# Kernel optimization log

Hardware: AMD Instinct MI355X
Metric: run time of the kernel (lower is better)

Reference implementation:

```python
import jax, jax.numpy as jnp
import numpy as np

S, B, C, H, DH = 16, 16, 256, 4, 64
HW_TABLE, HW_HAND = 256, 36
HW = HW_TABLE + HW_HAND + 1  # 293 spatial tokens (table + hand + global)
LK = 128
MAX_T = 64
UH, UW, UC = 4, 4, 2
TH, TW, HH, HWW = 16, 16, 6, 6
N_MODES, N_SHAPES, N_COLORS = 20, 64, 16


def _ln(x, g, b):
    m = jnp.mean(x, -1, keepdims=True)
    v = jnp.var(x, -1, keepdims=True)
    return (x - m) / jnp.sqrt(v + 1e-5) * g + b


def _forward(tq, pad_q, xk, tk, pad_k,
             spatial_enc, temporal_enc, ln1_g, ln1_b,
             wq, bq, wk, bk, wv, bv, wo, bo, ln2_g, ln2_b,
             w1, b1, w2, b2, table_w, table_b, hand_w, hand_b,
             mode_w, mode_b, shape_w, shape_b, color_w, color_b):
    s, b = tq.shape
    Lq = s * HW
    # temporal + spatial positional broadcast-add -> padded query stream
    xt = temporal_enc[tq]                                        # (s,b,C)
    xq = (xt[:, None] + spatial_enc[None, :, None]).reshape(Lq, b, C)
    tq_e = jnp.broadcast_to(tq[:, None], (s, HW, b)).reshape(Lq, b)
    # padded causal mask: key visible iff tk <= tq, key in pad_k, query in pad_q*HW
    allowed = ((tk[None] <= tq_e[:, None])
               & (jnp.arange(LK)[None, :, None] < pad_k[None, None])
               & (jnp.arange(Lq)[:, None, None] < (pad_q * HW)[None, None]))  # (Lq,Lk,b)
    # cross-attention TransformerBlock (pre-LN MHA + FFN)
    qn = _ln(xq, ln1_g, ln1_b)
    Q = (qn @ wq + bq).reshape(Lq, b, H, DH)
    K = (xk @ wk + bk).reshape(LK, b, H, DH)
    V = (xk @ wv + bv).reshape(LK, b, H, DH)
    scores = jnp.einsum('qbhd,kbhd->bhqk', Q, K) / np.float32(np.sqrt(DH))
    scores = jnp.where(jnp.transpose(allowed, (2, 0, 1))[:, None], scores, jnp.float32(-1e9))
    a = jnp.einsum('bhqk,kbhd->qbhd', jax.nn.softmax(scores, -1), V).reshape(Lq, b, C)
    x = xq + a @ wo + bo
    x = x + jax.nn.gelu(_ln(x, ln2_g, ln2_b) @ w1 + b1) @ w2 + b2
    x = x.reshape(s, HW, b, C)
    # table decode: pixel-unshuffle (s,th,tw,b,uh,uw,uc) -> (s,b,uc,th*uh,tw*uw)
    tx = x[:, :HW_TABLE] @ table_w + table_b
    tx = tx.reshape(s, TH, TW, b, UH, UW, UC).transpose(0, 3, 6, 1, 4, 2, 5)
    tx = tx.reshape(s, b, UC, TH * UH, TW * UW)
    hx = x[:, HW_TABLE:HW_TABLE + HW_HAND] @ hand_w + hand_b
    hx = hx.reshape(s, HH, HWW, b, UH, UW, UC).transpose(0, 3, 6, 1, 4, 2, 5)
    hx = hx.reshape(s, b, UC, HH * UH, HWW * UW)
    gx = x[:, HW - 1]  # (s,b,C) global token
    return (gx @ mode_w + mode_b, gx @ shape_w + shape_b, gx @ color_w + color_b, tx, hx)


def setup_inputs():
    ks = jax.random.split(jax.random.key(0), 40)
    p = lambda k, shp: jax.random.normal(k, shp, jnp.float32) * 0.02
    inp = {}
    inp['tq'] = jnp.sort(jax.random.randint(ks[0], (S, B), 0, MAX_T), axis=0)
    inp['pad_q'] = jax.random.randint(ks[1], (B,), S // 2, S + 1)
    inp['xk'] = jax.random.normal(ks[2], (LK, B, C), jnp.float32)
    inp['tk'] = jnp.sort(jax.random.randint(ks[3], (LK, B), 0, MAX_T), axis=0).at[0].set(0)
    inp['pad_k'] = jax.random.randint(ks[4], (B,), LK // 2, LK + 1)
    inp['table_cursor_activate'] = jax.random.randint(ks[5], (S, B), 0, 2)
    inp['hand_cursor_activate'] = jax.random.randint(ks[6], (S, B), 0, 2)
    inp['insert_activate'] = jax.random.randint(ks[7], (S, B), 0, 2)
    inp['spatial_enc'] = p(ks[8], (HW, C))
    inp['temporal_enc'] = p(ks[9], (MAX_T, C))
    inp['ln1_g'] = jnp.ones(C); inp['ln1_b'] = jnp.zeros(C)
    inp['wq'] = p(ks[10], (C, C)); inp['bq'] = jnp.zeros(C)
    inp['wk'] = p(ks[11], (C, C)); inp['bk'] = jnp.zeros(C)
    inp['wv'] = p(ks[12], (C, C)); inp['bv'] = jnp.zeros(C)
    inp['wo'] = p(ks[13], (C, C)); inp['bo'] = jnp.zeros(C)
    inp['ln2_g'] = jnp.ones(C); inp['ln2_b'] = jnp.zeros(C)
    inp['w1'] = p(ks[14], (C, 4 * C)); inp['b1'] = jnp.zeros(4 * C)
    inp['w2'] = p(ks[15], (4 * C, C)); inp['b2'] = jnp.zeros(C)
    inp['table_w'] = p(ks[16], (C, UH * UW * UC)); inp['table_b'] = jnp.zeros(UH * UW * UC)
    inp['hand_w'] = p(ks[17], (C, UH * UW * UC)); inp['hand_b'] = jnp.zeros(UH * UW * UC)
    inp['mode_w'] = p(ks[18], (C, N_MODES)); inp['mode_b'] = jnp.zeros(N_MODES)
    inp['shape_w'] = p(ks[19], (C, N_SHAPES)); inp['shape_b'] = jnp.zeros(N_SHAPES)
    inp['color_w'] = p(ks[20], (C, N_COLORS)); inp['color_b'] = jnp.zeros(N_COLORS)
    return inp


def reference(tq, pad_q, xk, tk, pad_k, table_cursor_activate, hand_cursor_activate,
              insert_activate, spatial_enc, temporal_enc, ln1_g, ln1_b,
              wq, bq, wk, bk, wv, bv, wo, bo, ln2_g, ln2_b,
              w1, b1, w2, b2, table_w, table_b, hand_w, hand_b,
              mode_w, mode_b, shape_w, shape_b, color_w, color_b):
    # cursor/insert activates are unused in the old_style branch
    return _forward(tq, pad_q, xk, tk, pad_k, spatial_enc, temporal_enc,
                    ln1_g, ln1_b, wq, bq, wk, bk, wv, bv, wo, bo, ln2_g, ln2_b,
                    w1, b1, w2, b2, table_w, table_b, hand_w, hand_b,
                    mode_w, mode_b, shape_w, shape_b, color_w, color_b)
```

## Files before the change

### kernel.cpp

```cpp
#include <hip/hip_runtime.h>
#include <hip/hip_bf16.h>

namespace {
constexpr int cS = 16, cB = 16, cC = 256, cH = 4, cDH = 64, cHW = 293;
constexpr int cLQ = cS * cHW;
constexpr int cLK = 128;
constexpr int cNN = cLQ * cB;
constexpr size_t TX_OFF = 25600;
constexpr size_t HX_OFF = 2122752;
}

typedef unsigned short ushort_t;
typedef unsigned int uint_t;
typedef __attribute__((ext_vector_type(8))) short short8;
typedef __attribute__((ext_vector_type(4))) float f32x4;

__device__ __forceinline__ float bf2f(ushort_t u) {
  return __uint_as_float(((uint_t)u) << 16);
}
__device__ __forceinline__ ushort_t f2bf(float f) {
  __hip_bfloat16 h = __float2bfloat16(f);
  return *(ushort_t*)&h;
}

__device__ __forceinline__ size_t swz(int r, int c) {
  return (((size_t)(r >> 4) * 8 + (c >> 5)) * 64 + ((c >> 3) & 3) * 16 + (r & 15)) * 8 + (c & 7);
}

__global__ __launch_bounds__(256) void k_prep(
    const float* __restrict__ xk, ushort_t* __restrict__ xkb,
    const float* __restrict__ wq, ushort_t* __restrict__ wqs,
    const float* __restrict__ wk, ushort_t* __restrict__ wks,
    const float* __restrict__ wv, ushort_t* __restrict__ wvs,
    const float* __restrict__ wo, ushort_t* __restrict__ wos,
    const float* __restrict__ w1, ushort_t* __restrict__ w1s,
    const float* __restrict__ w2, ushort_t* __restrict__ w2s,
    const float* __restrict__ tw, ushort_t* __restrict__ tws,
    const float* __restrict__ hw_, ushort_t* __restrict__ hws)
{
  int bid = blockIdx.x;
  if (bid < 512) {
    int i4 = bid * 256 + threadIdx.x;
    int r = i4 >> 6;
    int c0 = (i4 & 63) * 4;
    float4 v = *(const float4*)(xk + (size_t)r * 256 + c0);
    ushort_t o[4] = {f2bf(v.x), f2bf(v.y), f2bf(v.z), f2bf(v.w)};
    *(uint2*)&xkb[swz(r, c0)] = *(uint2*)o;
    return;
  }
  int rr = bid - 512;
  const float* W; ushort_t* Ws; int N; int lb;
  if      (rr < 32)  { W = wq;  Ws = wqs; N = 256;  lb = rr; }
  else if (rr < 64)  { W = wk;  Ws = wks; N = 256;  lb = rr - 32; }
  else if (rr < 96)  { W = wv;  Ws = wvs; N = 256;  lb = rr - 64; }
  else if (rr < 128) { W = wo;  Ws = wos; N = 256;  lb = rr - 96; }
  else if (rr < 256) { W = w1;  Ws = w1s; N = 1024; lb = rr - 128; }
  else if (rr < 384) { W = w2;  Ws = w2s; N = 256;  lb = rr - 256; }
  else if (rr < 388) { W = tw;  Ws = tws; N = 32;   lb = rr - 384; }
  else               { W = hw_; Ws = hws; N = 32;   lb = rr - 388; }
  int slot = lb * 256 + threadIdx.x;
  int lane = slot & 63;
  int fr   = slot >> 6;
  int NB   = N >> 4;
  int nb   = fr % NB, kc = fr / NB;
  int n    = nb * 16 + (lane & 15);
  int k0   = kc * 32 + (lane >> 4) * 8;
  ushort_t tmp[8];
  #pragma unroll
  for (int i = 0; i < 8; ++i) tmp[i] = f2bf(W[(size_t)(k0 + i) * N + n]);
  *(uint4*)&Ws[(size_t)slot * 8] = *(uint4*)tmp;
}

__device__ __forceinline__ void gemm_k256(
    const ushort_t* __restrict__ A, const ushort_t* __restrict__ Ws,
    int rt0, int slot0, int NB, int lane, f32x4 c[4][4])
{
  #pragma unroll 2
  for (int kc = 0; kc < 8; ++kc) {
    short8 a[4];
    #pragma unroll
    for (int mf = 0; mf < 4; ++mf)
      a[mf] = *(const short8*)(A + (((size_t)(rt0 + mf) * 8 + kc) * 64 + lane) * 8);
    #pragma unroll
    for (int nb = 0; nb < 4; ++nb) {
      short8 b = *(const short8*)(Ws + (((size_t)kc * NB + slot0 + nb) * 64 + lane) * 8);
      #pragma unroll
      for (int mf = 0; mf < 4; ++mf)
        c[mf][nb] = __builtin_amdgcn_mfma_f32_16x16x32_bf16(a[mf], b, c[mf][nb], 0, 0, 0);
    }
  }
}

__global__ __launch_bounds__(256, 4) void k_qnp(
    const int* __restrict__ tq, const float* __restrict__ spatial,
    const float* __restrict__ temporal, const float* __restrict__ g,
    const float* __restrict__ bt, const ushort_t* __restrict__ Ws,
    const float* __restrict__ Bi, ushort_t* __restrict__ Out)
{
  __shared__ ushort_t aT[64 * 256];
  const int tid = threadIdx.x, lane = tid & 63, w = tid >> 6;
  const int rt0 = blockIdx.x * 4, row0 = blockIdx.x * 64;
  {
    int q = rt0 + w;
    int s = q / cHW, hw = q % cHW;
    int c0 = lane * 4;
    float4 sv = *(const float4*)(spatial + (size_t)hw * cC + c0);
    float4 g4 = *(const float4*)(g + c0);
    float4 b4 = *(const float4*)(bt + c0);
    int kc = c0 >> 5, qq = (c0 >> 3) & 3, joff = c0 & 7;
    for (int rr = 0; rr < 16; ++rr) {
      int t = tq[s * cB + rr];
      float4 tv = *(const float4*)(temporal + (size_t)t * cC + c0);
      float v0 = tv.x + sv.x, v1 = tv.y + sv.y, v2 = tv.z + sv.z, v3 = tv.w + sv.w;
      float sum = v0 + v1 + v2 + v3;
      float sum2 = v0 * v0 + v1 * v1 + v2 * v2 + v3 * v3;
      #pragma unroll
      for (int off = 32; off >= 1; off >>= 1) {
        sum  += __shfl_xor(sum,  off, 64);
        sum2 += __shfl_xor(sum2, off, 64);
      }
      float mean = sum * (1.0f / cC);
      float var  = sum2 * (1.0f / cC) - mean * mean;
      float inv  = rsqrtf(var + 1e-5f);
      ushort_t o[4] = {f2bf((v0 - mean) * inv * g4.x + b4.x),
                       f2bf((v1 - mean) * inv * g4.y + b4.y),
                       f2bf((v2 - mean) * inv * g4.z + b4.z),
                       f2bf((v3 - mean) * inv * g4.w + b4.w)};
      *(uint2*)&aT[(((w * 8 + kc) * 64) + qq * 16 + rr) * 8 + joff] = *(uint2*)o;
    }
  }
  __syncthreads();
  f32x4 z = {0.f, 0.f, 0.f, 0.f};
  f32x4 c[4][4];
  #pragma unroll
  for (int mf = 0; mf < 4; ++mf)
    #pragma unroll
    for (int nb = 0; nb < 4; ++nb) c[mf][nb] = z;
  gemm_k256(aT, Ws, 0, w * 4, 16, lane, c);
  const int lane15 = lane & 15, kq = lane >> 4;
  __syncthreads();
  #pragma unroll
  for (int nb = 0; nb < 4; ++nb) {
    int col = w * 64 + nb * 16 + lane15;
    float bias = Bi[col];
    #pragma unroll
    for (int mf = 0; mf < 4; ++mf)
      #pragma unroll
      for (int i = 0; i < 4; ++i)
        aT[(mf * 16 + kq * 4 + i) * 256 + col] = f2bf(c[mf][nb][i] + bias);
  }
  __syncthreads();
  uint2* outp = (uint2*)(Out + (size_t)row0 * 256);
  #pragma unroll
  for (int it = 0; it < 16; ++it) {
    int f = tid + it * 256;
    int row = f >> 6, c0 = (f & 63) * 4;
    outp[f] = *(uint2*)&aT[row * 256 + c0];
  }
}

__global__ __launch_bounds__(256, 4) void k_kv(
    const ushort_t* __restrict__ xkb, const ushort_t* __restrict__ wks,
    const ushort_t* __restrict__ wvs, const float* __restrict__ bk,
    const float* __restrict__ bv, ushort_t* __restrict__ Kb,
    ushort_t* __restrict__ Vb)
{
  const ushort_t* Ws = blockIdx.y ? wvs : wks;
  const float* Bi = blockIdx.y ? bv : bk;
  ushort_t* Out = blockIdx.y ? Vb : Kb;
  const int lane = threadIdx.x & 63, w = threadIdx.x >> 6;
  const int rt0 = blockIdx.x * 4, row0 = blockIdx.x * 64;
  f32x4 z = {0.f, 0.f, 0.f, 0.f};
  f32x4 c[4][4];
  #pragma unroll
  for (int mf = 0; mf < 4; ++mf)
    #pragma unroll
    for (int nb = 0; nb < 4; ++nb) c[mf][nb] = z;
  gemm_k256(xkb, Ws, rt0, w * 4, 16, lane, c);
  const int lane15 = lane & 15, kq = lane >> 4;
  #pragma unroll
  for (int nb = 0; nb < 4; ++nb) {
    int col = w * 64 + nb * 16 + lane15;
    float bias = Bi[col];
    #pragma unroll
    for (int mf = 0; mf < 4; ++mf)
      #pragma unroll
      for (int i = 0; i < 4; ++i) {
        int row = row0 + mf * 16 + kq * 4 + i;
        Out[(size_t)row * 256 + col] = f2bf(c[mf][nb][i] + bias);
      }
  }
}

__global__ __launch_bounds__(512, 4) void k_woffn(
    const ushort_t* __restrict__ A, const ushort_t* __restrict__ wos,
    const float* __restrict__ bo, const int* __restrict__ tq,
    const float* __restrict__ spatial, const float* __restrict__ temporal,
    const float* __restrict__ g, const float* __restrict__ bt,
    const ushort_t* __restrict__ w1s, const float* __restrict__ b1,
    const ushort_t* __restrict__ w2s, const float* __restrict__ b2,
    ushort_t* xres, ushort_t* __restrict__ x2out)
{
  __shared__ ushort_t aT[64 * 256];
  __shared__ ushort_t hL[64 * 256];
  __shared__ float red[8][64][2];
  __shared__ float meanL[64], invL[64];
  const int tid = threadIdx.x, lane = tid & 63, w = tid >> 6;
  const int lane15 = lane & 15, kq = lane >> 4;
  const int rt0 = blockIdx.x * 4, row0 = blockIdx.x * 64;
  const f32x4 z = {0.f, 0.f, 0.f, 0.f};

  f32x4 c[4][2];
  #pragma unroll
  for (int mf = 0; mf < 4; ++mf)
    #pragma unroll
    for (int nb = 0; nb < 2; ++nb) c[mf][nb] = z;
  #pragma unroll 1
  for (int kc = 0; kc < 8; ++kc) {
    short8 a[4];
    #pragma unroll
    for (int mf = 0; mf < 4; ++mf)
      a[mf] = *(const short8*)(A + (((size_t)(rt0 + mf) * 8 + kc) * 64 + lane) * 8);
    #pragma unroll
    for (int nb = 0; nb < 2; ++nb) {
      short8 b = *(const short8*)(wos + (((size_t)kc * 16 + w * 2 + nb) * 64 + lane) * 8);
      #pragma unroll
      for (int mf = 0; mf < 4; ++mf)
        c[mf][nb] = __builtin_amdgcn_mfma_f32_16x16x32_bf16(a[mf], b, c[mf][nb], 0, 0, 0);
    }
  }
  {
    int tt[4][4], hws[4];
    #pragma unroll
    for (int mf = 0; mf < 4; ++mf) {
      int q = rt0 + mf;
      int s = q / cHW;
      hws[mf] = q % cHW;
      #pragma unroll
      for (int i = 0; i < 4; ++i) tt[mf][i] = tq[s * cB + kq * 4 + i];
    }
    #pragma unroll
    for (int nb = 0; nb < 2; ++nb) {
      int col = w * 32 + nb * 16 + lane15;
      float bias = bo[col];
      #pragma unroll
      for (int mf = 0; mf < 4; ++mf) {
        float sp = spatial[(size_t)hws[mf] * cC + col];
        #pragma unroll
        for (int i = 0; i < 4; ++i)
          c[mf][nb][i] += bias + temporal[(size_t)tt[mf][i] * cC + col] + sp;
      }
    }
  }
  #pragma unroll
  for (int mf = 0; mf < 4; ++mf)
    #pragma unroll
    for (int i = 0; i < 4; ++i) {
      float s4 = c[mf][0][i] + c[mf][1][i];
      float q4 = c[mf][0][i] * c[mf][0][i] + c[mf][1][i] * c[mf][1][i];
      #pragma unroll
      for (int off = 8; off >= 1; off >>= 1) {
        s4 += __shfl_xor(s4, off, 64);
        q4 += __shfl_xor(q4, off, 64);
      }
      if (lane15 == 0) {
        red[w][mf * 16 + kq * 4 + i][0] = s4;
        red[w][mf * 16 + kq * 4 + i][1] = q4;
      }
    }
  __syncthreads();
  if (tid < 64) {
    float S = 0.f, Q = 0.f;
    #pragma unroll
    for (int ww = 0; ww < 8; ++ww) { S += red[ww][tid][0]; Q += red[ww][tid][1]; }
    float m = S * (1.0f / cC);
    float v = Q * (1.0f / cC) - m * m;
    meanL[tid] = m;
    invL[tid] = rsqrtf(v + 1e-5f);
  }
  __syncthreads();
  #pragma unroll
  for (int nb = 0; nb < 2; ++nb) {
    int col = w * 32 + nb * 16 + lane15;
    float gc = g[col], bc = bt[col];
    int qd = nb * 2 + (lane15 >> 3);
    int jd = lane15 & 7;
    #pragma unroll
    for (int mf = 0; mf < 4; ++mf)
      #pragma unroll
      for (int i = 0; i < 4; ++i) {
        int rl = mf * 16 + kq * 4 + i;
        float val = c[mf][nb][i];
        float lv = (val - meanL[rl]) * invL[rl] * gc + bc;
        aT[((mf * 8 + w) * 64 + qd * 16 + kq * 4 + i) * 8 + jd] = f2bf(lv);
        hL[rl * 256 + col] = f2bf(val);
      }
  }
  __syncthreads();
  {
    uint2* xw = (uint2*)(xres + (size_t)row0 * 256);
    #pragma unroll
    for (int it = 0; it < 8; ++it) {
      int f = tid + it * 512;
      int row = f >> 6, c0 = (f & 63) * 4;
      xw[f] = *(uint2*)&hL[row * 256 + c0];
    }
  }
  f32x4 c2[4][2];
  #pragma unroll
  for (int mf = 0; mf < 4; ++mf)
    #pragma unroll
    for (int nb = 0; nb < 2; ++nb) c2[mf][nb] = z;
  for (int hc = 0; hc < 4; ++hc) {
    #pragma unroll
    for (int half = 0; half < 2; ++half) {
      f32x4 c1[4];
      #pragma unroll
      for (int mf = 0; mf < 4; ++mf) c1[mf] = z;
      #pragma unroll 1
      for (int kc = 0; kc < 8; ++kc) {
        short8 a[4];
        #pragma unroll
        for (int mf = 0; mf < 4; ++mf)
          a[mf] = *(const short8*)&aT[((mf * 8 + kc) * 64 + lane) * 8];
        int slot = hc * 16 + w * 2 + half;
        short8 b = *(const short8*)(w1s + (((size_t)kc * 64 + slot) * 64 + lane) * 8);
        #pragma unroll
        for (int mf = 0; mf < 4; ++mf)
          c1[mf] = __builtin_amdgcn_mfma_f32_16x16x32_bf16(a[mf], b, c1[mf], 0, 0, 0);
      }
      if (half == 0) __syncthreads();
      {
        int k2l = w * 32 + half * 16 + lane15;
        float bias = b1[hc * 256 + k2l];
        int kc2l = k2l >> 5, kq2 = (k2l >> 3) & 3, j2 = k2l & 7;
        #pragma unroll
        for (int mf = 0; mf < 4; ++mf)
          #pragma unroll
          for (int i = 0; i < 4; ++i) {
            float xx = c1[mf][i] + bias;
            float x2v = xx * xx;
            float mm = fmaf(x2v, 0.044715f, 1.0f);
            float u2 = xx * mm * -1.5957691216057308f;
            float e = __expf(u2);
            float ge = xx * __builtin_amdgcn_rcpf(1.0f + e);
            hL[(((kc2l * 4 + mf) * 64) + kq2 * 16 + kq * 4 + i) * 8 + j2] = f2bf(ge);
          }
      }
    }
    __syncthreads();
    #pragma unroll 1
    for (int kc2 = 0; kc2 < 8; ++kc2) {
      short8 a2[4];
      #pragma unroll
      for (int mf = 0; mf < 4; ++mf)
        a2[mf] = *(const short8*)&hL[((kc2 * 4 + mf) * 64 + lane) * 8];
      #pragma unroll
      for (int nb = 0; nb < 2; ++nb) {
        short8 b = *(const short8*)(w2s +
            (((size_t)(hc * 8 + kc2) * 16 + w * 2 + nb) * 64 + lane) * 8);
        #pragma unroll
        for (int mf = 0; mf < 4; ++mf)
          c2[mf][nb] = __builtin_amdgcn_mfma_f32_16x16x32_bf16(a2[mf], b, c2[mf][nb], 0, 0, 0);
      }
    }
  }
  __syncthreads();
  #pragma unroll
  for (int nb = 0; nb < 2; ++nb) {
    int col = w * 32 + nb * 16 + lane15;
    float bias = b2[col];
    #pragma unroll
    for (int mf = 0; mf < 4; ++mf)
      #pragma unroll
      for (int i = 0; i < 4; ++i)
        aT[(mf * 16 + kq * 4 + i) * 256 + col] = f2bf(c2[mf][nb][i] + bias);
  }
  __syncthreads();
  {
    const int rt = (tid + 256) & 511;
    uint2* xp = (uint2*)(x2out + (size_t)row0 * 256);
    const uint2* xr = (const uint2*)(xres + (size_t)row0 * 256);
    #pragma unroll
    for (int it = 0; it < 8; ++it) {
      int f = rt + it * 512;
      int row = f >> 6, c0 = (f & 63) * 4;
      uint2 hv = *(uint2*)&aT[row * 256 + c0];
      uint2 rv = xr[f];
      const ushort_t* hp = (const ushort_t*)&hv;
      const ushort_t* rp = (const ushort_t*)&rv;
      ushort_t o[4];
      #pragma unroll
      for (int j = 0; j < 4; ++j) o[j] = f2bf(bf2f(hp[j]) + bf2f(rp[j]));
      xp[f] = *(uint2*)o;
    }
  }
}

__global__ __launch_bounds__(512, 4) void k_attn(
    const ushort_t* __restrict__ Qb, const ushort_t* __restrict__ Kb,
    const ushort_t* __restrict__ Vb, const int* __restrict__ tq,
    const int* __restrict__ tk, const int* __restrict__ pad_q,
    const int* __restrict__ pad_k, ushort_t* __restrict__ aout)
{
  __shared__ ushort_t KL[128 * 72];
  __shared__ ushort_t VtL[64 * 136];
  __shared__ ushort_t pL[8][16 * 136];
  __shared__ int tkL[128];

  const int h = blockIdx.y, b = blockIdx.z;
  const int tid = threadIdx.x, lane = tid & 63, w = tid >> 6;
  const int m15 = lane & 15, quad = lane >> 4;

  for (int i = tid; i < 128 * 16; i += 512) {
    int k = i >> 4, d4 = (i & 15) * 4;
    size_t src = (size_t)(k * cB + b) * 256 + h * 64 + d4;
    uint2 kv = *(const uint2*)&Kb[src];
    uint2 vv = *(const uint2*)&Vb[src];
    *(uint2*)&KL[k * 72 + d4] = kv;
    const ushort_t* vvp = (const ushort_t*)&vv;
    #pragma unroll
    for (int t = 0; t < 4; ++t) VtL[(d4 + t) * 136 + k] = vvp[t];
  }
  if (tid < 128) tkL[tid] = tk[tid * cB + b];
  __syncthreads();
  const int pk = pad_k[b];
  const int pq = pad_q[b] * cHW;
  ushort_t* pRow = pL[w];
  const f32x4 z = {0.f, 0.f, 0.f, 0.f};

  for (int pr = 0; pr < 4; ++pr) {
    int qt = blockIdx.x * 32 + pr * 8 + w;
    if (qt >= 293) break;
    const ushort_t* qrow =
        Qb + ((size_t)((qt * 16 + m15) * cB + b)) * 256 + h * 64 + quad * 8;
    short8 qa0 = *(const short8*)(qrow);
    short8 qa1 = *(const short8*)(qrow + 32);
    f32x4 s[8];
    #pragma unroll
    for (int nf = 0; nf < 8; ++nf) {
      const ushort_t* kp = KL + (nf * 16 + m15) * 72 + quad * 8;
      short8 b0 = *(const short8*)(kp);
      short8 b1 = *(const short8*)(kp + 32);
      s[nf] = __builtin_amdgcn_mfma_f32_16x16x32_bf16(qa0, b0, z, 0, 0, 0);
      s[nf] = __builtin_amdgcn_mfma_f32_16x16x32_bf16(qa1, b1, s[nf], 0, 0, 0);
    }
    int tqv[4], qok[4];
    #pragma unroll
    for (int i = 0; i < 4; ++i) {
      int qg = qt * 16 + quad * 4 + i;
      int sidx = (qg * 3579) >> 20;
      tqv[i] = tq[sidx * cB + b];
      qok[i] = (qg < pq);
    }
    #pragma unroll
    for (int nf = 0; nf < 8; ++nf) {
      int kidx = nf * 16 + m15;
      int tkc = tkL[kidx];
      bool kok = (kidx < pk);
      #pragma unroll
      for (int i = 0; i < 4; ++i) {
        bool ok = kok && qok[i] && (tkc <= tqv[i]);
        s[nf][i] = ok ? s[nf][i] * 0.125f : -1e9f;
      }
    }
    float mx[4], l[4];
    #pragma unroll
    for (int i = 0; i < 4; ++i) {
      float m = s[0][i];
      #pragma unroll
      for (int nf = 1; nf < 8; ++nf) m = fmaxf(m, s[nf][i]);
      #pragma unroll
      for (int off = 8; off >= 1; off >>= 1) m = fmaxf(m, __shfl_xor(m, off, 64));
      mx[i] = m;
    }
    #pragma unroll
    for (int i = 0; i < 4; ++i) l[i] = 0.f;
    #pragma unroll
    for (int nf = 0; nf < 8; ++nf)
      #pragma unroll
      for (int i = 0; i < 4; ++i) {
        float p = __expf(s[nf][i] - mx[i]);
        s[nf][i] = p;
        l[i] += p;
      }
    #pragma unroll
    for (int i = 0; i < 4; ++i) {
      float t = l[i];
      #pragma unroll
      for (int off = 8; off >= 1; off >>= 1) t += __shfl_xor(t, off, 64);
      l[i] = 1.0f / t;
    }
    #pragma unroll
    for (int nf = 0; nf < 8; ++nf)
      #pragma unroll
      for (int i = 0; i < 4; ++i)
        pRow[(quad * 4 + i) * 136 + nf * 16 + m15] = f2bf(s[nf][i]);
    f32x4 o[4];
    #pragma unroll
    for (int nf = 0; nf < 4; ++nf) o[nf] = z;
    #pragma unroll
    for (int kc = 0; kc < 4; ++kc) {
      short8 pa = *(const short8*)(pRow + m15 * 136 + kc * 32 + quad * 8);
      #pragma unroll
      for (int nf = 0; nf < 4; ++nf) {
        short8 vb = *(const short8*)(VtL + (nf * 16 + m15) * 136 + kc * 32 + quad * 8);
        o[nf] = __builtin_amdgcn_mfma_f32_16x16x32_bf16(pa, vb, o[nf], 0, 0, 0);
      }
    }
    #pragma unroll
    for (int nf = 0; nf < 4; ++nf) {
      int c = h * 64 + nf * 16 + m15;
      size_t base = ((size_t)(c >> 5)) * 64 + ((c >> 3) & 3) * 16 + b;
      int cj = c & 7;
      #pragma unroll
      for (int i = 0; i < 4; ++i) {
        int qg = qt * 16 + quad * 4 + i;
        aout[(((size_t)qg * 8) * 64 + base) * 8 + cj] = f2bf(o[nf][i] * l[i]);
      }
    }
  }
}

__global__ __launch_bounds__(256, 4) void k_thg(
    const ushort_t* __restrict__ x2, const ushort_t* __restrict__ tws,
    const float* __restrict__ tb, const ushort_t* __restrict__ hws,
    const float* __restrict__ hb,
    const float* __restrict__ mw, const float* __restrict__ mbi,
    const float* __restrict__ sw, const float* __restrict__ sbi,
    const float* __restrict__ cw, const float* __restrict__ cbi,
    float* __restrict__ out)
{
  __shared__ ushort_t aT[64 * 264];
  const int NTH = cNN / 64;
  const int tid = threadIdx.x;
  if ((int)blockIdx.x >= NTH) {
    int sb = blockIdx.x - NTH;
    int s = sb >> 4, b = sb & 15;
    float* rowL = (float*)aT;
    const ushort_t* row = x2 + ((size_t)(s * cHW + 292) * cB + b) * cC;
    if (tid < 256) rowL[tid] = bf2f(row[tid]);
    __syncthreads();
    int j = tid;
    if (j < 100) {
      const float* W;
      const float* Bi;
      int jj, M;
      size_t off;
      if (j < 20)      { W = mw; Bi = mbi; jj = j;      M = 20; off = 0;     }
      else if (j < 84) { W = sw; Bi = sbi; jj = j - 20; M = 64; off = 5120;  }
      else             { W = cw; Bi = cbi; jj = j - 84; M = 16; off = 21504; }
      float acc = Bi[jj];
      for (int c = 0; c < 256; ++c) acc = fmaf(rowL[c], W[c * M + jj], acc);
      out[off + (size_t)sb * M + jj] = acc;
    }
    return;
  }
  const int lane = tid & 63, w = tid >> 6;
  const int m15 = lane & 15, quad = lane >> 4;
  const int row0 = blockIdx.x * 64;
  #pragma unroll
  for (int it = 0; it < 8; ++it) {
    int f = tid + it * 256;
    int row = f >> 5, cb = f & 31;
    *(uint4*)&aT[row * 264 + cb * 8] =
        *(const uint4*)&x2[(size_t)(row0 + row) * 256 + cb * 8];
  }
  __syncthreads();
  const f32x4 z = {0.f, 0.f, 0.f, 0.f};
  f32x4 ct[2], ch[2];
  ct[0] = ct[1] = ch[0] = ch[1] = z;
  const ushort_t* arow = aT + (w * 16 + m15) * 264 + quad * 8;
  #pragma unroll
  for (int kc = 0; kc < 8; ++kc) {
    short8 a = *(const short8*)(arow + kc * 32);
    #pragma unroll
    for (int nb = 0; nb < 2; ++nb) {
      short8 bt_ = *(const short8*)(tws + (((size_t)(kc * 2 + nb)) * 64 + lane) * 8);
      short8 bh_ = *(const short8*)(hws + (((size_t)(kc * 2 + nb)) * 64 + lane) * 8);
      ct[nb] = __builtin_amdgcn_mfma_f32_16x16x32_bf16(a, bt_, ct[nb], 0, 0, 0);
      ch[nb] = __builtin_amdgcn_mfma_f32_16x16x32_bf16(a, bh_, ch[nb], 0, 0, 0);
    }
  }
  #pragma unroll
  for (int nb = 0; nb < 2; ++nb) {
    int j = nb * 16 + m15;
    float tbias = tb[j], hbias = hb[j];
    int uh = j >> 3, uw = (j >> 1) & 3, uc = j & 1;
    #pragma unroll
    for (int i = 0; i < 4; ++i) {
      int rg = row0 + w * 16 + quad * 4 + i;
      int b = rg & 15, q = rg >> 4;
      int s = (q * 3579) >> 20;
      int hw = q - s * cHW;
      if (hw < 256) {
        int th = hw >> 4, twi = hw & 15;
        size_t idx = TX_OFF +
            ((((size_t)(s * cB + b)) * 2 + uc) * 64 + (th * 4 + uh)) * 64 + (twi * 4 + uw);
        out[idx] = ct[nb][i] + tbias;
      } else if (hw < 292) {
        int h2 = hw - 256;
        int hh = h2 / 6, ww = h2 % 6;
        size_t idx = HX_OFF +
            ((((size_t)(s * cB + b)) * 2 + uc) * 24 + (hh * 4 + uh)) * 24 + (ww * 4 + uw);
        out[idx] = ch[nb][i] + hbias;
      }
    }
  }
}

extern "C" void kernel_launch(void* const* d_in, const int* in_sizes, int n_in,
                              void* d_out, int out_size, void* d_ws, size_t ws_size,
                              hipStream_t stream)
{
  const int*   tq       = (const int*)d_in[0];
  const int*   pad_q    = (const int*)d_in[1];
  const float* xk       = (const float*)d_in[2];
  const int*   tk       = (const int*)d_in[3];
  const int*   pad_k    = (const int*)d_in[4];
  const float* spatial  = (const float*)d_in[8];
  const float* temporal = (const float*)d_in[9];
  const float* ln1_g    = (const float*)d_in[10];
  const float* ln1_b    = (const float*)d_in[11];
  const float* wq       = (const float*)d_in[12];
  const float* bq       = (const float*)d_in[13];
  const float* wk       = (const float*)d_in[14];
  const float* bk       = (const float*)d_in[15];
  const float* wv       = (const float*)d_in[16];
  const float* bv       = (const float*)d_in[17];
  const float* wo       = (const float*)d_in[18];
  const float* bo       = (const float*)d_in[19];
  const float* ln2_g    = (const float*)d_in[20];
  const float* ln2_b    = (const float*)d_in[21];
  const float* w1       = (const float*)d_in[22];
  const float* b1       = (const float*)d_in[23];
  const float* w2       = (const float*)d_in[24];
  const float* b2       = (const float*)d_in[25];
  const float* table_w  = (const float*)d_in[26];
  const float* table_b  = (const float*)d_in[27];
  const float* hand_w   = (const float*)d_in[28];
  const float* hand_b   = (const float*)d_in[29];
  const float* mode_w   = (const float*)d_in[30];
  const float* mode_b   = (const float*)d_in[31];
  const float* shape_w  = (const float*)d_in[32];
  const float* shape_b  = (const float*)d_in[33];
  const float* color_w  = (const float*)d_in[34];
  const float* color_b  = (const float*)d_in[35];
  float* out = (float*)d_out;

  char* ws = (char*)d_ws;
  const size_t NB2 = (size_t)cNN * cC * sizeof(ushort_t);
  ushort_t* buf1 = (ushort_t*)ws;
  ushort_t* buf2 = (ushort_t*)(ws + NB2);
  char* p = ws + 2 * NB2;
  ushort_t* Kb  = (ushort_t*)p;  p += (size_t)cLK * cB * 256 * 2;
  ushort_t* Vb  = (ushort_t*)p;  p += (size_t)cLK * cB * 256 * 2;
  ushort_t* xkb = (ushort_t*)p;  p += (size_t)cLK * cB * 256 * 2;
  ushort_t* wqs = (ushort_t*)p;  p += 256 * 256 * 2;
  ushort_t* wks = (ushort_t*)p;  p += 256 * 256 * 2;
  ushort_t* wvs = (ushort_t*)p;  p += 256 * 256 * 2;
  ushort_t* wos = (ushort_t*)p;  p += 256 * 256 * 2;
  ushort_t* w1s = (ushort_t*)p;  p += 256 * 1024 * 2;
  ushort_t* w2s = (ushort_t*)p;  p += 1024 * 256 * 2;
  ushort_t* tws = (ushort_t*)p;  p += 256 * 32 * 2;
  ushort_t* hws = (ushort_t*)p;  p += 256 * 32 * 2;

  k_prep<<<904, 256, 0, stream>>>(xk, xkb, wq, wqs, wk, wks, wv, wvs,
                                  wo, wos, w1, w1s, w2, w2s,
                                  table_w, tws, hand_w, hws);
  k_kv<<<dim3(32, 2), 256, 0, stream>>>(xkb, wks, wvs, bk, bv, Kb, Vb);
  k_qnp<<<cNN / 64, 256, 0, stream>>>(tq, spatial, temporal, ln1_g, ln1_b,
                                      wqs, bq, buf2);
  k_attn<<<dim3(10, cH, cB), 512, 0, stream>>>(buf2, Kb, Vb, tq, tk,
                                               pad_q, pad_k, buf1);
  k_woffn<<<cNN / 64, 512, 0, stream>>>(buf1, wos, bo, tq, spatial, temporal,
                                        ln2_g, ln2_b, w1s, b1, w2s, b2,
                                        buf1, buf2);
  k_thg<<<cNN / 64 + cS * cB, 256, 0, stream>>>(buf2, tws, table_b, hws, hand_b,
                                                mode_w, mode_b, shape_w, shape_b,
                                                color_w, color_b, out);
}
```

Measured before the change: 417.9 us.

## Fuse table/hand decode into FFN kernel and split attention grid finer

The table/hand projection GEMM and pixel-unshuffle scatter now run at the end of the Wo+FFN kernel, reusing the final residual tile already held in shared memory. This removes a full re-read of the x2 activation buffer and one tile-loading pass. The global-token heads move to a small separate kernel. Separately, the attention grid doubles its x dimension (each block handles 16 query tiles instead of 32) to expose more parallelism, at the cost of reloading K/V per block.

```diff
diff --git a/kernel.cpp b/kernel.cpp
--- a/kernel.cpp
+++ b/kernel.cpp
@@ -199,7 +199,9 @@
     const float* __restrict__ g, const float* __restrict__ bt,
     const ushort_t* __restrict__ w1s, const float* __restrict__ b1,
     const ushort_t* __restrict__ w2s, const float* __restrict__ b2,
-    ushort_t* xres, ushort_t* __restrict__ x2out)
+    const ushort_t* __restrict__ tws, const float* __restrict__ tb,
+    const ushort_t* __restrict__ hws, const float* __restrict__ hb,
+    ushort_t* xres, ushort_t* __restrict__ x2out, float* __restrict__ hout)
 {
   __shared__ ushort_t aT[64 * 256];
   __shared__ ushort_t hL[64 * 256];
@@ -230,12 +232,12 @@
     }
   }
   {
-    int tt[4][4], hws[4];
+    int tt[4][4], hws_[4];
     #pragma unroll
     for (int mf = 0; mf < 4; ++mf) {
       int q = rt0 + mf;
       int s = q / cHW;
-      hws[mf] = q % cHW;
+      hws_[mf] = q % cHW;
       #pragma unroll
       for (int i = 0; i < 4; ++i) tt[mf][i] = tq[s * cB + kq * 4 + i];
     }
@@ -245,7 +247,7 @@
       float bias = bo[col];
       #pragma unroll
       for (int mf = 0; mf < 4; ++mf) {
-        float sp = spatial[(size_t)hws[mf] * cC + col];
+        float sp = spatial[(size_t)hws_[mf] * cC + col];
         #pragma unroll
         for (int i = 0; i < 4; ++i)
           c[mf][nb][i] += bias + temporal[(size_t)tt[mf][i] * cC + col] + sp;
@@ -393,6 +395,49 @@
       #pragma unroll
       for (int j = 0; j < 4; ++j) o[j] = f2bf(bf2f(hp[j]) + bf2f(rp[j]));
       xp[f] = *(uint2*)o;
+      *(uint2*)&aT[row * 256 + c0] = *(uint2*)o;
+    }
+  }
+  __syncthreads();
+  if (w < 4) {
+    f32x4 ct[2], ch[2];
+    ct[0] = ct[1] = ch[0] = ch[1] = z;
+    const ushort_t* arow = aT + (w * 16 + lane15) * 256 + kq * 8;
+    #pragma unroll
+    for (int kc = 0; kc < 8; ++kc) {
+      short8 a = *(const short8*)(arow + kc * 32);
+      #pragma unroll
+      for (int nb = 0; nb < 2; ++nb) {
+        short8 bt_ = *(const short8*)(tws + (((size_t)(kc * 2 + nb)) * 64 + lane) * 8);
+        short8 bh_ = *(const short8*)(hws + (((size_t)(kc * 2 + nb)) * 64 + lane) * 8);
+        ct[nb] = __builtin_amdgcn_mfma_f32_16x16x32_bf16(a, bt_, ct[nb], 0, 0, 0);
+        ch[nb] = __builtin_amdgcn_mfma_f32_16x16x32_bf16(a, bh_, ch[nb], 0, 0, 0);
+      }
+    }
+    #pragma unroll
+    for (int nb = 0; nb < 2; ++nb) {
+      int j = nb * 16 + lane15;
+      float tbias = tb[j], hbias = hb[j];
+      int uh = j >> 3, uw = (j >> 1) & 3, uc = j & 1;
+      #pragma unroll
+      for (int i = 0; i < 4; ++i) {
+        int rg = row0 + w * 16 + kq * 4 + i;
+        int b = rg & 15, q = rg >> 4;
+        int s = (q * 3579) >> 20;
+        int hw = q - s * cHW;
+        if (hw < 256) {
+          int th = hw >> 4, twi = hw & 15;
+          size_t idx = TX_OFF +
+              ((((size_t)(s * cB + b)) * 2 + uc) * 64 + (th * 4 + uh)) * 64 + (twi * 4 + uw);
+          hout[idx] = ct[nb][i] + tbias;
+        } else if (hw < 292) {
+          int h2 = hw - 256;
+          int hh = h2 / 6, ww = h2 % 6;
+          size_t idx = HX_OFF +
+              ((((size_t)(s * cB + b)) * 2 + uc) * 24 + (hh * 4 + uh)) * 24 + (ww * 4 + uw);
+          hout[idx] = ch[nb][i] + hbias;
+        }
+      }
     }
   }
 }
@@ -429,8 +474,8 @@
   ushort_t* pRow = pL[w];
   const f32x4 z = {0.f, 0.f, 0.f, 0.f};
 
-  for (int pr = 0; pr < 4; ++pr) {
-    int qt = blockIdx.x * 32 + pr * 8 + w;
+  for (int pr = 0; pr < 2; ++pr) {
+    int qt = blockIdx.x * 16 + pr * 8 + w;
     if (qt >= 293) break;
     const ushort_t* qrow =
         Qb + ((size_t)((qt * 16 + m15) * cB + b)) * 256 + h * 64 + quad * 8;
@@ -522,90 +567,31 @@
   }
 }
 
-__global__ __launch_bounds__(256, 4) void k_thg(
-    const ushort_t* __restrict__ x2, const ushort_t* __restrict__ tws,
-    const float* __restrict__ tb, const ushort_t* __restrict__ hws,
-    const float* __restrict__ hb,
+__global__ __launch_bounds__(128) void k_gx(
+    const ushort_t* __restrict__ x2,
     const float* __restrict__ mw, const float* __restrict__ mbi,
     const float* __restrict__ sw, const float* __restrict__ sbi,
     const float* __restrict__ cw, const float* __restrict__ cbi,
     float* __restrict__ out)
 {
-  __shared__ ushort_t aT[64 * 264];
-  const int NTH = cNN / 64;
-  const int tid = threadIdx.x;
-  if ((int)blockIdx.x >= NTH) {
-    int sb = blockIdx.x - NTH;
-    int s = sb >> 4, b = sb & 15;
-    float* rowL = (float*)aT;
-    const ushort_t* row = x2 + ((size_t)(s * cHW + 292) * cB + b) * cC;
-    if (tid < 256) rowL[tid] = bf2f(row[tid]);
-    __syncthreads();
-    int j = tid;
-    if (j < 100) {
-      const float* W;
-      const float* Bi;
-      int jj, M;
-      size_t off;
-      if (j < 20)      { W = mw; Bi = mbi; jj = j;      M = 20; off = 0;     }
-      else if (j < 84) { W = sw; Bi = sbi; jj = j - 20; M = 64; off = 5120;  }
-      else             { W = cw; Bi = cbi; jj = j - 84; M = 16; off = 21504; }
-      float acc = Bi[jj];
-      for (int c = 0; c < 256; ++c) acc = fmaf(rowL[c], W[c * M + jj], acc);
-      out[off + (size_t)sb * M + jj] = acc;
-    }
-    return;
-  }
-  const int lane = tid & 63, w = tid >> 6;
-  const int m15 = lane & 15, quad = lane >> 4;
-  const int row0 = blockIdx.x * 64;
-  #pragma unroll
-  for (int it = 0; it < 8; ++it) {
-    int f = tid + it * 256;
-    int row = f >> 5, cb = f & 31;
-    *(uint4*)&aT[row * 264 + cb * 8] =
-        *(const uint4*)&x2[(size_t)(row0 + row) * 256 + cb * 8];
-  }
-  __syncthreads();
-  const f32x4 z = {0.f, 0.f, 0.f, 0.f};
-  f32x4 ct[2], ch[2];
-  ct[0] = ct[1] = ch[0] = ch[1] = z;
-  const ushort_t* arow = aT + (w * 16 + m15) * 264 + quad * 8;
-  #pragma unroll
-  for (int kc = 0; kc < 8; ++kc) {
-    short8 a = *(const short8*)(arow + kc * 32);
-    #pragma unroll
-    for (int nb = 0; nb < 2; ++nb) {
-      short8 bt_ = *(const short8*)(tws + (((size_t)(kc * 2 + nb)) * 64 + lane) * 8);
-      short8 bh_ = *(const short8*)(hws + (((size_t)(kc * 2 + nb)) * 64 + lane) * 8);
-      ct[nb] = __builtin_amdgcn_mfma_f32_16x16x32_bf16(a, bt_, ct[nb], 0, 0, 0);
-      ch[nb] = __builtin_amdgcn_mfma_f32_16x16x32_bf16(a, bh_, ch[nb], 0, 0, 0);
-    }
-  }
-  #pragma unroll
-  for (int nb = 0; nb < 2; ++nb) {
-    int j = nb * 16 + m15;
-    float tbias = tb[j], hbias = hb[j];
-    int uh = j >> 3, uw = (j >> 1) & 3, uc = j & 1;
-    #pragma unroll
-    for (int i = 0; i < 4; ++i) {
-      int rg = row0 + w * 16 + quad * 4 + i;
-      int b = rg & 15, q = rg >> 4;
-      int s = (q * 3579) >> 20;
-      int hw = q - s * cHW;
-      if (hw < 256) {
-        int th = hw >> 4, twi = hw & 15;
-        size_t idx = TX_OFF +
-            ((((size_t)(s * cB + b)) * 2 + uc) * 64 + (th * 4 + uh)) * 64 + (twi * 4 + uw);
-        out[idx] = ct[nb][i] + tbias;
-      } else if (hw < 292) {
-        int h2 = hw - 256;
-        int hh = h2 / 6, ww = h2 % 6;
-        size_t idx = HX_OFF +
-            ((((size_t)(s * cB + b)) * 2 + uc) * 24 + (hh * 4 + uh)) * 24 + (ww * 4 + uw);
-        out[idx] = ch[nb][i] + hbias;
-      }
-    }
+  int sb = blockIdx.x;
+  int s = sb >> 4, b = sb & 15;
+  __shared__ float rowL[256];
+  const ushort_t* row = x2 + ((size_t)(s * cHW + 292) * cB + b) * cC;
+  for (int i = threadIdx.x; i < 256; i += 128) rowL[i] = bf2f(row[i]);
+  __syncthreads();
+  int j = threadIdx.x;
+  if (j < 100) {
+    const float* W;
+    const float* Bi;
+    int jj, M;
+    size_t off;
+    if (j < 20)      { W = mw; Bi = mbi; jj = j;      M = 20; off = 0;     }
+    else if (j < 84) { W = sw; Bi = sbi; jj = j - 20; M = 64; off = 5120;  }
+    else             { W = cw; Bi = cbi; jj = j - 84; M = 16; off = 21504; }
+    float acc = Bi[jj];
+    for (int c = 0; c < 256; ++c) acc = fmaf(rowL[c], W[c * M + jj], acc);
+    out[off + (size_t)sb * M + jj] = acc;
   }
 }
 
@@ -671,12 +657,12 @@
   k_kv<<<dim3(32, 2), 256, 0, stream>>>(xkb, wks, wvs, bk, bv, Kb, Vb);
   k_qnp<<<cNN / 64, 256, 0, stream>>>(tq, spatial, temporal, ln1_g, ln1_b,
                                       wqs, bq, buf2);
-  k_attn<<<dim3(10, cH, cB), 512, 0, stream>>>(buf2, Kb, Vb, tq, tk,
+  k_attn<<<dim3(19, cH, cB), 512, 0, stream>>>(buf2, Kb, Vb, tq, tk,
                                                pad_q, pad_k, buf1);
   k_woffn<<<cNN / 64, 512, 0, stream>>>(buf1, wos, bo, tq, spatial, temporal,
                                         ln2_g, ln2_b, w1s, b1, w2s, b2,
-                                        buf1, buf2);
-  k_thg<<<cNN / 64 + cS * cB, 256, 0, stream>>>(buf2, tws, table_b, hws, hand_b,
-                                                mode_w, mode_b, shape_w, shape_b,
-                                                color_w, color_b, out);
-}
+                                        tws, table_b, hws, hand_b,
+                                        buf1, buf2, out);
+  k_gx<<<cS * cB, 128, 0, stream>>>(buf2, mode_w, mode_b, shape_w, shape_b,
+                                    color_w, color_b, out);
+}
```

After: 427.7 us. 2.3% more time.
